# Kernel optimization log

Hardware: AMD Instinct MI355X
Metric: run time of the kernel (lower is better)

Reference implementation:

```python
import jax, jax.numpy as jnp
import numpy as np

N_NODES = 40000
N_EDGES = 640000
IN_CH = 11
HID = 128
OUT_CH = 1
NUM_LEVELS = 2


def _lin(x, w, b):
    # torch nn.Linear: w is [out, in]
    return x @ w.T + b


def _conv(x, src, dst, w1, b1, w2, b2, w3, b3):
    # Reconstructed MLMPNNConv forward: embed, then NUM_LEVELS rounds of
    # scatter-add message passing (message = x_j), concat levels, project.
    h = jax.nn.relu(_lin(x, w1, b1))  # [N, HID]
    outs = []
    for _ in range(NUM_LEVELS):
        agg = jax.ops.segment_sum(h[src], dst, num_segments=N_NODES)  # gather + scatter-add
        h = jax.nn.relu(_lin(agg, w2, b2))
        outs.append(h)
    return _lin(jnp.concatenate(outs, axis=-1), w3, b3)  # [N, out]


def setup_inputs() -> dict:
    key = jax.random.key(0)
    ks = jax.random.split(key, 16)
    d = {}
    d["x"] = jax.random.normal(ks[0], (N_NODES, IN_CH), dtype=jnp.float32)
    d["edge_index"] = jax.random.randint(ks[1], (2, N_EDGES), 0, N_NODES, dtype=jnp.int32)
    s = 0.05
    # conv 0: lin1 IN->HID, lin2 HID->HID, lin3 2*HID->HID
    d["c0_w1"] = jax.random.normal(ks[2], (HID, IN_CH)) * s
    d["c0_b1"] = jnp.zeros((HID,), jnp.float32)
    d["c0_w2"] = jax.random.normal(ks[3], (HID, HID)) * s
    d["c0_b2"] = jnp.zeros((HID,), jnp.float32)
    d["c0_w3"] = jax.random.normal(ks[4], (HID, HID * NUM_LEVELS)) * s
    d["c0_b3"] = jnp.zeros((HID,), jnp.float32)
    # conv 1: lin1 HID->HID
    d["c1_w1"] = jax.random.normal(ks[5], (HID, HID)) * s
    d["c1_b1"] = jnp.zeros((HID,), jnp.float32)
    d["c1_w2"] = jax.random.normal(ks[6], (HID, HID)) * s
    d["c1_b2"] = jnp.zeros((HID,), jnp.float32)
    d["c1_w3"] = jax.random.normal(ks[7], (HID, HID * NUM_LEVELS)) * s
    d["c1_b3"] = jnp.zeros((HID,), jnp.float32)
    # head
    d["f_w1"] = jax.random.normal(ks[8], (HID, HID)) * s
    d["f_b1"] = jnp.zeros((HID,), jnp.float32)
    d["f_w2"] = jax.random.normal(ks[9], (OUT_CH, HID)) * s
    d["f_b2"] = jnp.zeros((OUT_CH,), jnp.float32)
    return d


def reference(x, edge_index,
              c0_w1, c0_b1, c0_w2, c0_b2, c0_w3, c0_b3,
              c1_w1, c1_b1, c1_w2, c1_b2, c1_w3, c1_b3,
              f_w1, f_b1, f_w2, f_b2):
    src, dst = edge_index[0], edge_index[1]
    h = _conv(x, src, dst, c0_w1, c0_b1, c0_w2, c0_b2, c0_w3, c0_b3)
    h = _conv(h, src, dst, c1_w1, c1_b1, c1_w2, c1_b2, c1_w3, c1_b3)
    h = jax.nn.relu(_lin(h, f_w1, f_b1))
    return _lin(h, f_w2, f_b2)  # [N, 1]
```

## Files before the change

### kernel.cpp

```cpp
#include <hip/hip_runtime.h>
#include <hip/hip_fp16.h>

#define NN 40000
#define NE 640000
#define HID 128
#define SCAN_BLK ((NN + 255) / 256)
#define EB ((NE + 255) / 256)
#define ECAP 1536

typedef __attribute__((ext_vector_type(8)))  short short8;
typedef __attribute__((ext_vector_type(4)))  short short4v;
typedef __attribute__((ext_vector_type(16))) float floatx16;
typedef unsigned int uint;

__device__ __forceinline__ short f2bf(float f) {
    union { float f; unsigned u; } c; c.f = f;
    unsigned u = c.u;
    unsigned r = (u + 0x7FFF + ((u >> 16) & 1)) >> 16;
    return (short)r;
}
__device__ __forceinline__ float bf2f(short h) {
    union { unsigned u; float f; } c;
    c.u = ((unsigned)(unsigned short)h) << 16;
    return c.f;
}
__device__ __forceinline__ float2 h2f2(uint u) {
    union { uint u; __half2 h; } c; c.u = u;
    return __half22float2(c.h);
}
__device__ __forceinline__ void splits(float f, short* hi, short* lo) {
    short h = f2bf(f);
    *hi = h;
    *lo = f2bf(f - bf2f(h));
}
__device__ __forceinline__ void unpack8(uint4 a, uint4 b, short8* h, short8* l) {
    short8 H, L;
    H[0] = (short)(a.x >> 16); L[0] = (short)a.x;
    H[1] = (short)(a.y >> 16); L[1] = (short)a.y;
    H[2] = (short)(a.z >> 16); L[2] = (short)a.z;
    H[3] = (short)(a.w >> 16); L[3] = (short)a.w;
    H[4] = (short)(b.x >> 16); L[4] = (short)b.x;
    H[5] = (short)(b.y >> 16); L[5] = (short)b.y;
    H[6] = (short)(b.z >> 16); L[6] = (short)b.z;
    H[7] = (short)(b.w >> 16); L[7] = (short)b.w;
    *h = H; *l = L;
}

__device__ __forceinline__ int wswz(int o, int k) {
    int chunk = k >> 4, half = (k >> 3) & 1, j = k & 7;
    int ct = o >> 5, m31 = o & 31;
    int lane = half * 32 + m31;
    return (((chunk * 4 + ct) * 64 + lane) * 8 + j);
}

#define ACC4(u, A, B)                                                     \
    { float2 f0 = h2f2(u.x), f1 = h2f2(u.y);                              \
      float2 f2 = h2f2(u.z), f3 = h2f2(u.w);                              \
      A.x += f0.x; A.y += f0.y; A.z += f1.x; A.w += f1.y;                 \
      B.x += f2.x; B.y += f2.y; B.z += f3.x; B.w += f3.y; }

#define GBODY(IDX)                                                        \
        for (; e + 8 <= hi; e += 8) {                                     \
            int s0 = IDX(e + sub);     int s1 = IDX(e + 2 + sub);         \
            int s2 = IDX(e + 4 + sub); int s3 = IDX(e + 6 + sub);         \
            uint4 u0 = hp[(size_t)s0 * 16 + c16];                         \
            uint4 u1 = hp[(size_t)s1 * 16 + c16];                         \
            uint4 u2 = hp[(size_t)s2 * 16 + c16];                         \
            uint4 u3 = hp[(size_t)s3 * 16 + c16];                         \
            ACC4(u0, a0, a1); ACC4(u1, b0, b1);                           \
            ACC4(u2, c0, c1); ACC4(u3, d0, d1);                           \
        }                                                                 \
        for (; e + 2 <= hi; e += 2) {                                     \
            int s0 = IDX(e + sub);                                        \
            uint4 u0 = hp[(size_t)s0 * 16 + c16];                         \
            ACC4(u0, a0, a1);                                             \
        }                                                                 \
        if (sub == 0 && e < hi) {                                         \
            int s0 = IDX(e);                                              \
            uint4 u0 = hp[(size_t)s0 * 16 + c16];                         \
            ACC4(u0, b0, b1);                                             \
        }

#define IDXS(j) sE[(j)]
#define IDXG(j) esrc[lo0 + (j)]

__global__ __launch_bounds__(256, 4) void fused_gather_lin_kernel(
    const __half* __restrict__ h, const int* __restrict__ row_ptr,
    const int* __restrict__ esrc, const uint* __restrict__ Wq,
    const float* __restrict__ bias, __half* __restrict__ out)
{
    __shared__ short sAh[4096];
    __shared__ short sAl[4096];
    __shared__ int   sE[ECAP];
    __shared__ int   sRP[33];
    __shared__ int   sCtr;
    const int t   = threadIdx.x;
    const int r0  = blockIdx.x * 32;
    const int c16 = t & 15;
    const int sub = (t >> 4) & 1;
    const uint4* hp = (const uint4*)h;

    if (t == 0) sCtr = 0;
    if (t < 33) sRP[t] = row_ptr[r0 + t];
    __syncthreads();
    const int lo0 = sRP[0];
    const int nE  = sRP[32] - lo0;
    const int nStage = nE < ECAP ? nE : ECAP;
    for (int i = t; i < nStage; i += 256) sE[i] = esrc[lo0 + i];
    __syncthreads();
    const bool fast = (nE <= ECAP);

    for (;;) {
        int n = 0;
        if ((t & 31) == 0) n = atomicAdd(&sCtr, 1);
        n = __shfl(n, 0, 32);
        if (n >= 32) break;
        const int lo = sRP[n] - lo0, hi = sRP[n + 1] - lo0;
        float4 a0 = make_float4(0,0,0,0), a1 = make_float4(0,0,0,0);
        float4 b0 = make_float4(0,0,0,0), b1 = make_float4(0,0,0,0);
        float4 c0 = make_float4(0,0,0,0), c1 = make_float4(0,0,0,0);
        float4 d0 = make_float4(0,0,0,0), d1 = make_float4(0,0,0,0);
        int e = lo;
        if (fast) { GBODY(IDXS) } else { GBODY(IDXG) }
        float4 v0, v1;
        v0.x = (a0.x + b0.x) + (c0.x + d0.x);
        v0.y = (a0.y + b0.y) + (c0.y + d0.y);
        v0.z = (a0.z + b0.z) + (c0.z + d0.z);
        v0.w = (a0.w + b0.w) + (c0.w + d0.w);
        v1.x = (a1.x + b1.x) + (c1.x + d1.x);
        v1.y = (a1.y + b1.y) + (c1.y + d1.y);
        v1.z = (a1.z + b1.z) + (c1.z + d1.z);
        v1.w = (a1.w + b1.w) + (c1.w + d1.w);
        v0.x += __shfl_down(v0.x, 16, 32);
        v0.y += __shfl_down(v0.y, 16, 32);
        v0.z += __shfl_down(v0.z, 16, 32);
        v0.w += __shfl_down(v0.w, 16, 32);
        v1.x += __shfl_down(v1.x, 16, 32);
        v1.y += __shfl_down(v1.y, 16, 32);
        v1.z += __shfl_down(v1.z, 16, 32);
        v1.w += __shfl_down(v1.w, 16, 32);
        if (sub == 0) {
            short8 H, L;
            short hh, ll;
            splits(v0.x, &hh, &ll); H[0] = hh; L[0] = ll;
            splits(v0.y, &hh, &ll); H[1] = hh; L[1] = ll;
            splits(v0.z, &hh, &ll); H[2] = hh; L[2] = ll;
            splits(v0.w, &hh, &ll); H[3] = hh; L[3] = ll;
            splits(v1.x, &hh, &ll); H[4] = hh; L[4] = ll;
            splits(v1.y, &hh, &ll); H[5] = hh; L[5] = ll;
            splits(v1.z, &hh, &ll); H[6] = hh; L[6] = ll;
            splits(v1.w, &hh, &ll); H[7] = hh; L[7] = ll;
            const int off = c16 * 256 + n * 8;
            *(short8*)(sAh + off) = H;
            *(short8*)(sAl + off) = L;
        }
    }
    __syncthreads();

    const int wv   = t >> 6;
    const int lane = t & 63;
    const int m31  = lane & 31;
    const int half = lane >> 5;
    floatx16 acc;
    #pragma unroll
    for (int i = 0; i < 16; ++i) acc[i] = 0.f;
    #pragma unroll
    for (int c = 0; c < 8; ++c) {
        short8 ah = *(const short8*)(sAh + (c * 2 + half) * 256 + m31 * 8);
        short8 al = *(const short8*)(sAl + (c * 2 + half) * 256 + m31 * 8);
        const uint* wr = Wq + ((size_t)(c * 4 + wv) * 64 + lane) * 8;
        uint4 w0 = *(const uint4*)(wr);
        uint4 w1 = *(const uint4*)(wr + 4);
        short8 bh, bl;
        unpack8(w0, w1, &bh, &bl);
        acc = __builtin_amdgcn_mfma_f32_32x32x16_bf16(ah, bh, acc, 0, 0, 0);
        acc = __builtin_amdgcn_mfma_f32_32x32x16_bf16(al, bh, acc, 0, 0, 0);
        acc = __builtin_amdgcn_mfma_f32_32x32x16_bf16(ah, bl, acc, 0, 0, 0);
    }
    const int col = wv * 32 + m31;
    const float bb = bias[col];
    #pragma unroll
    for (int reg = 0; reg < 16; ++reg) {
        int row = (reg & 3) + 8 * (reg >> 2) + 4 * half;
        float v = fmaxf(acc[reg] + bb, 0.f);
        out[(size_t)(r0 + row) * HID + col] = __float2half(v);
    }
}

template<int PHASES, bool RELU>
__global__ __launch_bounds__(256, 4) void lin32_kernel(
    const __half* __restrict__ X0, const __half* __restrict__ X1,
    const uint* __restrict__ Wq, const float* __restrict__ bias,
    __half* __restrict__ out)
{
    __shared__ short sAh[PHASES * 4096];
    __shared__ short sAl[PHASES * 4096];
    const int t  = threadIdx.x;
    const int r0 = blockIdx.x * 32;

    #pragma unroll
    for (int i = 0; i < PHASES * 4; ++i) {
        int v = t + 256 * i;
        const __half* Xp = (PHASES == 2 && v >= 1024) ? X1 : X0;
        int vv  = v & 1023;
        int row = vv >> 5, q = vv & 31;
        uint2 u = *(const uint2*)(Xp + (size_t)(r0 + row) * 128 + q * 4);
        float2 f0 = h2f2(u.x), f1 = h2f2(u.y);
        int kk  = ((PHASES == 2) ? (v >> 10) * 128 : 0) + q * 4;
        int off = (kk >> 3) * 256 + row * 8 + (q & 1) * 4;
        short4v hi, lo;
        short hh, ll;
        splits(f0.x, &hh, &ll); hi.x = hh; lo.x = ll;
        splits(f0.y, &hh, &ll); hi.y = hh; lo.y = ll;
        splits(f1.x, &hh, &ll); hi.z = hh; lo.z = ll;
        splits(f1.y, &hh, &ll); hi.w = hh; lo.w = ll;
        *(short4v*)(sAh + off) = hi;
        *(short4v*)(sAl + off) = lo;
    }
    __syncthreads();

    const int wv   = t >> 6;
    const int lane = t & 63;
    const int m31  = lane & 31;
    const int half = lane >> 5;
    floatx16 acc;
    #pragma unroll
    for (int i = 0; i < 16; ++i) acc[i] = 0.f;
    #pragma unroll
    for (int c = 0; c < PHASES * 8; ++c) {
        short8 ah = *(const short8*)(sAh + (c * 2 + half) * 256 + m31 * 8);
        short8 al = *(const short8*)(sAl + (c * 2 + half) * 256 + m31 * 8);
        const uint* wr = Wq + ((size_t)(c * 4 + wv) * 64 + lane) * 8;
        uint4 w0 = *(const uint4*)(wr);
        uint4 w1 = *(const uint4*)(wr + 4);
        short8 bh, bl;
        unpack8(w0, w1, &bh, &bl);
        acc = __builtin_amdgcn_mfma_f32_32x32x16_bf16(ah, bh, acc, 0, 0, 0);
        acc = __builtin_amdgcn_mfma_f32_32x32x16_bf16(al, bh, acc, 0, 0, 0);
        acc = __builtin_amdgcn_mfma_f32_32x32x16_bf16(ah, bl, acc, 0, 0, 0);
    }
    const int col = wv * 32 + m31;
    const float bb = bias[col];
    #pragma unroll
    for (int reg = 0; reg < 16; ++reg) {
        int row = (reg & 3) + 8 * (reg >> 2) + 4 * half;
        float v = acc[reg] + bb;
        if (RELU) v = fmaxf(v, 0.f);
        out[(size_t)(r0 + row) * HID + col] = __float2half(v);
    }
}

__global__ __launch_bounds__(256, 3) void cat_head_kernel(
    const __half* __restrict__ X0, const __half* __restrict__ X1,
    const uint* __restrict__ Wq, const float* __restrict__ bias,
    const float* __restrict__ f2, const float* __restrict__ f2b,
    float* __restrict__ out)
{
    __shared__ short sAh[8192];
    __shared__ short sAl[8192];
    __shared__ float gbuf[32 * 129];
    const int t  = threadIdx.x;
    const int r0 = blockIdx.x * 32;

    #pragma unroll
    for (int i = 0; i < 8; ++i) {
        int v = t + 256 * i;
        const __half* Xp = (v >= 1024) ? X1 : X0;
        int vv  = v & 1023;
        int row = vv >> 5, q = vv & 31;
        uint2 u = *(const uint2*)(Xp + (size_t)(r0 + row) * 128 + q * 4);
        float2 f0 = h2f2(u.x), f1 = h2f2(u.y);
        int kk  = (v >> 10) * 128 + q * 4;
        int off = (kk >> 3) * 256 + row * 8 + (q & 1) * 4;
        short4v hi, lo;
        short hh, ll;
        splits(f0.x, &hh, &ll); hi.x = hh; lo.x = ll;
        splits(f0.y, &hh, &ll); hi.y = hh; lo.y = ll;
        splits(f1.x, &hh, &ll); hi.z = hh; lo.z = ll;
        splits(f1.y, &hh, &ll); hi.w = hh; lo.w = ll;
        *(short4v*)(sAh + off) = hi;
        *(short4v*)(sAl + off) = lo;
    }
    __syncthreads();

    const int wv   = t >> 6;
    const int lane = t & 63;
    const int m31  = lane & 31;
    const int half = lane >> 5;
    floatx16 acc;
    #pragma unroll
    for (int i = 0; i < 16; ++i) acc[i] = 0.f;
    #pragma unroll
    for (int c = 0; c < 16; ++c) {
        short8 ah = *(const short8*)(sAh + (c * 2 + half) * 256 + m31 * 8);
        short8 al = *(const short8*)(sAl + (c * 2 + half) * 256 + m31 * 8);
        const uint* wr = Wq + ((size_t)(c * 4 + wv) * 64 + lane) * 8;
        uint4 w0 = *(const uint4*)(wr);
        uint4 w1 = *(const uint4*)(wr + 4);
        short8 bh, bl;
        unpack8(w0, w1, &bh, &bl);
        acc = __builtin_amdgcn_mfma_f32_32x32x16_bf16(ah, bh, acc, 0, 0, 0);
        acc = __builtin_amdgcn_mfma_f32_32x32x16_bf16(al, bh, acc, 0, 0, 0);
        acc = __builtin_amdgcn_mfma_f32_32x32x16_bf16(ah, bl, acc, 0, 0, 0);
    }
    const int col = wv * 32 + m31;
    const float bb = bias[col];
    #pragma unroll
    for (int reg = 0; reg < 16; ++reg) {
        int row = (reg & 3) + 8 * (reg >> 2) + 4 * half;
        gbuf[row * 129 + col] = fmaxf(acc[reg] + bb, 0.f);
    }
    __syncthreads();

    const int node = t >> 3;
    const int seg  = t & 7;
    const float* gr = gbuf + node * 129 + seg * 16;
    float a = 0.f;
    #pragma unroll
    for (int i = 0; i < 16; ++i) a += gr[i] * f2[seg * 16 + i];
    a += __shfl_down(a, 4, 8);
    a += __shfl_down(a, 2, 8);
    a += __shfl_down(a, 1, 8);
    if (seg == 0) out[r0 + node] = a + f2b[0];
}

__global__ __launch_bounds__(256) void prep_kernel(
    const float* __restrict__ c0w2, const float* __restrict__ c1w2,
    const float* __restrict__ c1w1, const float* __restrict__ c0w3,
    const float* __restrict__ c0b3, const float* __restrict__ c1b1,
    const float* __restrict__ fw1,  const float* __restrict__ c1w3,
    const float* __restrict__ c1b3, const float* __restrict__ fb1,
    const int* __restrict__ dst, int* __restrict__ cnt,
    uint* __restrict__ wp, uint* __restrict__ p_Wa, uint* __restrict__ p_Wb,
    float* __restrict__ f_ba, float* __restrict__ f_bb)
{
    const int b = blockIdx.x;
    const int t = threadIdx.x;
    if (b < 128) {
        int i = b * 256 + t;
        const float* src = (i < 16384) ? c0w2 : c1w2;
        int off = (i < 16384) ? 0 : 16384;
        int L = i - off;
        int o = L >> 7, k = L & 127;
        short hh, ll;
        splits(src[L], &hh, &ll);
        wp[off + wswz(o, k)] = ((uint)(unsigned short)hh << 16) | (uint)(unsigned short)ll;
    } else if (b < 384) {
        const bool isA = (b < 256);
        const int o = b - (isA ? 128 : 256);
        const float* A   = isA ? c1w1 : fw1;
        const float* B   = isA ? c0w3 : c1w3;
        const float* bi  = isA ? c0b3 : c1b3;
        const float* bo  = isA ? c1b1 : fb1;
        uint*  W  = isA ? p_Wa : p_Wb;
        float* bb = isA ? f_ba : f_bb;
        const float* Ar = A + o * 128;
        float s = 0.f;
        for (int j = 0; j < 128; ++j) s += Ar[j] * B[j * 256 + t];
        short hh, ll;
        splits(s, &hh, &ll);
        W[wswz(o, t)] = ((uint)(unsigned short)hh << 16) | (uint)(unsigned short)ll;
        if (t == 0) {
            float sb = 0.f;
            for (int j = 0; j < 128; ++j) sb += Ar[j] * bi[j];
            bb[o] = sb + bo[o];
        }
    } else {
        int e = (b - 384) * 256 + t;
        if (e < NE) atomicAdd(&cnt[dst[e]], 1);
    }
}

__global__ __launch_bounds__(256) void scan1_kernel(
    const int* __restrict__ cnt, int* __restrict__ row_ptr,
    int* __restrict__ partials)
{
    __shared__ int s[256];
    const int t = threadIdx.x;
    const int i = blockIdx.x * 256 + t;
    int v = (i < NN) ? cnt[i] : 0;
    s[t] = v;
    __syncthreads();
    #pragma unroll
    for (int off = 1; off < 256; off <<= 1) {
        int x = (t >= off) ? s[t - off] : 0;
        __syncthreads();
        s[t] += x;
        __syncthreads();
    }
    if (i < NN) row_ptr[i] = s[t] - v;
    if (t == 255) partials[blockIdx.x] = s[255];
}

__global__ __launch_bounds__(256) void scan2_kernel(
    int* __restrict__ partials, int* __restrict__ row_ptr)
{
    __shared__ int s[256];
    const int t = threadIdx.x;
    int v = (t < SCAN_BLK) ? partials[t] : 0;
    s[t] = v;
    __syncthreads();
    #pragma unroll
    for (int off = 1; off < 256; off <<= 1) {
        int x = (t >= off) ? s[t - off] : 0;
        __syncthreads();
        s[t] += x;
        __syncthreads();
    }
    if (t < SCAN_BLK) partials[t] = s[t] - v;
    if (t == 255) row_ptr[NN] = s[255];
}

__global__ __launch_bounds__(256) void scan3_kernel(
    int* __restrict__ row_ptr, const int* __restrict__ partials)
{
    const int i = blockIdx.x * 256 + threadIdx.x;
    if (i < NN) row_ptr[i] += partials[blockIdx.x];
}

__global__ __launch_bounds__(256) void fill_embed_kernel(
    const int* __restrict__ src, const int* __restrict__ dst,
    const int* __restrict__ row_ptr, int* __restrict__ pos,
    int* __restrict__ esrc,
    const float* __restrict__ x, const float* __restrict__ w1,
    const float* __restrict__ b1, __half* __restrict__ h0)
{
    const int b = blockIdx.x;
    const int t = threadIdx.x;
    if (b < EB) {
        int e = b * 256 + t;
        if (e < NE) {
            int d = dst[e];
            int p = row_ptr[d] + atomicAdd(&pos[d], 1);
            esrc[p] = src[e];
        }
    } else {
        __shared__ float xs[2][88];
        const int hf = t >> 7;
        const int m  = t & 127;
        const int r0 = (b - EB) * 16 + hf * 8;
        for (int i = m; i < 88; i += 128) {
            int r = i / 11, k = i - r * 11;
            xs[hf][i] = x[(size_t)(r0 + r) * 11 + k];
        }
        __syncthreads();
        float acc[8] = {};
        const float* Wm = w1 + m * 11;
        #pragma unroll
        for (int k = 0; k < 11; ++k) {
            float w = Wm[k];
            #pragma unroll
            for (int r = 0; r < 8; ++r) acc[r] += xs[hf][r * 11 + k] * w;
        }
        const float bias = b1[m];
        #pragma unroll
        for (int r = 0; r < 8; ++r) {
            float v = fmaxf(acc[r] + bias, 0.f);
            h0[(size_t)(r0 + r) * HID + m] = __float2half(v);
        }
    }
}

extern "C" void kernel_launch(void* const* d_in, const int* in_sizes, int n_in,
                              void* d_out, int out_size, void* d_ws, size_t ws_size,
                              hipStream_t stream)
{
    const float* x     = (const float*)d_in[0];
    const int*   eidx  = (const int*)d_in[1];
    const float* c0_w1 = (const float*)d_in[2],  *c0_b1 = (const float*)d_in[3];
    const float* c0_w2 = (const float*)d_in[4],  *c0_b2 = (const float*)d_in[5];
    const float* c0_w3 = (const float*)d_in[6],  *c0_b3 = (const float*)d_in[7];
    const float* c1_w1 = (const float*)d_in[8],  *c1_b1 = (const float*)d_in[9];
    const float* c1_w2 = (const float*)d_in[10], *c1_b2 = (const float*)d_in[11];
    const float* c1_w3 = (const float*)d_in[12], *c1_b3 = (const float*)d_in[13];
    const float* f_w1  = (const float*)d_in[14], *f_b1  = (const float*)d_in[15];
    const float* f_w2  = (const float*)d_in[16], *f_b2  = (const float*)d_in[17];
    const int* src = eidx;
    const int* dst = eidx + NE;
    float* out = (float*)d_out;

    const size_t BUF = (size_t)NN * HID;
    __half* bA = (__half*)d_ws;
    __half* bB = bA + BUF;
    __half* bC = bB + BUF;
    int* row_ptr  = (int*)(bC + BUF);
    int* cnt      = row_ptr + (NN + 1);
    int* pos      = cnt + NN;
    int* esrc     = pos + NN;
    int* partials = esrc + NE;
    uint* wp      = (uint*)(partials + SCAN_BLK);

    uint* p_c0w2 = wp + 0;
    uint* p_c1w2 = wp + 16384;
    uint* p_Wa   = wp + 32768;
    uint* p_Wb   = wp + 65536;
    float* f_ba  = (float*)(wp + 98304);
    float* f_bb  = f_ba + 128;

    const int nbl = (NN + 31) / 32;

    (void)hipMemsetAsync(cnt, 0, 2 * NN * sizeof(int), stream);
    prep_kernel<<<384 + EB, 256, 0, stream>>>(
        c0_w2, c1_w2, c1_w1, c0_w3, c0_b3, c1_b1,
        f_w1, c1_w3, c1_b3, f_b1, dst, cnt, wp, p_Wa, p_Wb, f_ba, f_bb);
    scan1_kernel<<<SCAN_BLK, 256, 0, stream>>>(cnt, row_ptr, partials);
    scan2_kernel<<<1, 256, 0, stream>>>(partials, row_ptr);
    scan3_kernel<<<SCAN_BLK, 256, 0, stream>>>(row_ptr, partials);
    fill_embed_kernel<<<EB + 2500, 256, 0, stream>>>(
        src, dst, row_ptr, pos, esrc, x, c0_w1, c0_b1, bA);

    fused_gather_lin_kernel<<<nbl, 256, 0, stream>>>(bA, row_ptr, esrc, p_c0w2, c0_b2, bB);
    fused_gather_lin_kernel<<<nbl, 256, 0, stream>>>(bB, row_ptr, esrc, p_c0w2, c0_b2, bC);
    lin32_kernel<2, true><<<nbl, 256, 0, stream>>>(bB, bC, p_Wa, f_ba, bA);

    fused_gather_lin_kernel<<<nbl, 256, 0, stream>>>(bA, row_ptr, esrc, p_c1w2, c1_b2, bB);
    fused_gather_lin_kernel<<<nbl, 256, 0, stream>>>(bB, row_ptr, esrc, p_c1w2, c1_b2, bC);
    cat_head_kernel<<<nbl, 256, 0, stream>>>(bB, bC, p_Wb, f_bb, f_w2, f_b2, out);
}
```

Baseline: 306.5 us.

## Merge three-pass scan into one block and record edge rank during counting

The three-kernel scan over node degrees becomes a single 1024-thread block scan, where each thread serially sums a chunk of 40 counts. The counting pass also stores the atomicAdd return value as a per-edge rank, so the CSR fill no longer needs a second atomic per edge or the pos array. This removes two kernel launches, one memset region and 640K contended atomics. In exchange it adds a 640K-int rank write and read, aliased into the bC buffer, and a serial single-block scan with strided, uncoalesced per-thread reads.

```diff
diff --git a/kernel.cpp b/kernel.cpp
--- a/kernel.cpp
+++ b/kernel.cpp
@@ -4,7 +4,6 @@
 #define NN 40000
 #define NE 640000
 #define HID 128
-#define SCAN_BLK ((NN + 255) / 256)
 #define EB ((NE + 255) / 256)
 #define ECAP 1536
 
@@ -330,7 +329,7 @@
     const float* __restrict__ c0b3, const float* __restrict__ c1b1,
     const float* __restrict__ fw1,  const float* __restrict__ c1w3,
     const float* __restrict__ c1b3, const float* __restrict__ fb1,
-    const int* __restrict__ dst, int* __restrict__ cnt,
+    const int* __restrict__ dst, int* __restrict__ cnt, int* __restrict__ rank,
     uint* __restrict__ wp, uint* __restrict__ p_Wa, uint* __restrict__ p_Wb,
     float* __restrict__ f_ba, float* __restrict__ f_bb)
 {
@@ -367,60 +366,47 @@
         }
     } else {
         int e = (b - 384) * 256 + t;
-        if (e < NE) atomicAdd(&cnt[dst[e]], 1);
-    }
-}
-
-__global__ __launch_bounds__(256) void scan1_kernel(
-    const int* __restrict__ cnt, int* __restrict__ row_ptr,
-    int* __restrict__ partials)
-{
-    __shared__ int s[256];
+        if (e < NE) rank[e] = atomicAdd(&cnt[dst[e]], 1);
+    }
+}
+
+#define SCHUNK 40
+__global__ __launch_bounds__(1024) void scan_kernel(
+    const int* __restrict__ cnt, int* __restrict__ row_ptr)
+{
+    __shared__ int s[1024];
     const int t = threadIdx.x;
-    const int i = blockIdx.x * 256 + t;
-    int v = (i < NN) ? cnt[i] : 0;
-    s[t] = v;
-    __syncthreads();
-    #pragma unroll
-    for (int off = 1; off < 256; off <<= 1) {
+    const int base = t * SCHUNK;
+    int sum = 0;
+    if (base < NN) {
+        int n = min(SCHUNK, NN - base);
+        #pragma unroll 8
+        for (int j = 0; j < n; ++j) sum += cnt[base + j];
+    }
+    s[t] = sum;
+    __syncthreads();
+    #pragma unroll
+    for (int off = 1; off < 1024; off <<= 1) {
         int x = (t >= off) ? s[t - off] : 0;
         __syncthreads();
         s[t] += x;
         __syncthreads();
     }
-    if (i < NN) row_ptr[i] = s[t] - v;
-    if (t == 255) partials[blockIdx.x] = s[255];
-}
-
-__global__ __launch_bounds__(256) void scan2_kernel(
-    int* __restrict__ partials, int* __restrict__ row_ptr)
-{
-    __shared__ int s[256];
-    const int t = threadIdx.x;
-    int v = (t < SCAN_BLK) ? partials[t] : 0;
-    s[t] = v;
-    __syncthreads();
-    #pragma unroll
-    for (int off = 1; off < 256; off <<= 1) {
-        int x = (t >= off) ? s[t - off] : 0;
-        __syncthreads();
-        s[t] += x;
-        __syncthreads();
-    }
-    if (t < SCAN_BLK) partials[t] = s[t] - v;
-    if (t == 255) row_ptr[NN] = s[255];
-}
-
-__global__ __launch_bounds__(256) void scan3_kernel(
-    int* __restrict__ row_ptr, const int* __restrict__ partials)
-{
-    const int i = blockIdx.x * 256 + threadIdx.x;
-    if (i < NN) row_ptr[i] += partials[blockIdx.x];
+    int run = (t == 0) ? 0 : s[t - 1];
+    if (base < NN) {
+        int n = min(SCHUNK, NN - base);
+        for (int j = 0; j < n; ++j) {
+            int v = cnt[base + j];
+            row_ptr[base + j] = run;
+            run += v;
+        }
+    }
+    if (t == 1023) row_ptr[NN] = s[1023];
 }
 
 __global__ __launch_bounds__(256) void fill_embed_kernel(
     const int* __restrict__ src, const int* __restrict__ dst,
-    const int* __restrict__ row_ptr, int* __restrict__ pos,
+    const int* __restrict__ row_ptr, const int* __restrict__ rank,
     int* __restrict__ esrc,
     const float* __restrict__ x, const float* __restrict__ w1,
     const float* __restrict__ b1, __half* __restrict__ h0)
@@ -431,8 +417,7 @@
         int e = b * 256 + t;
         if (e < NE) {
             int d = dst[e];
-            int p = row_ptr[d] + atomicAdd(&pos[d], 1);
-            esrc[p] = src[e];
+            esrc[row_ptr[d] + rank[e]] = src[e];
         }
     } else {
         __shared__ float xs[2][88];
@@ -485,10 +470,8 @@
     __half* bC = bB + BUF;
     int* row_ptr  = (int*)(bC + BUF);
     int* cnt      = row_ptr + (NN + 1);
-    int* pos      = cnt + NN;
-    int* esrc     = pos + NN;
-    int* partials = esrc + NE;
-    uint* wp      = (uint*)(partials + SCAN_BLK);
+    int* esrc     = cnt + NN;
+    uint* wp      = (uint*)(esrc + NE);
 
     uint* p_c0w2 = wp + 0;
     uint* p_c1w2 = wp + 16384;
@@ -497,17 +480,17 @@
     float* f_ba  = (float*)(wp + 98304);
     float* f_bb  = f_ba + 128;
 
+    int* rank = (int*)bC;
+
     const int nbl = (NN + 31) / 32;
 
-    (void)hipMemsetAsync(cnt, 0, 2 * NN * sizeof(int), stream);
+    (void)hipMemsetAsync(cnt, 0, NN * sizeof(int), stream);
     prep_kernel<<<384 + EB, 256, 0, stream>>>(
         c0_w2, c1_w2, c1_w1, c0_w3, c0_b3, c1_b1,
-        f_w1, c1_w3, c1_b3, f_b1, dst, cnt, wp, p_Wa, p_Wb, f_ba, f_bb);
-    scan1_kernel<<<SCAN_BLK, 256, 0, stream>>>(cnt, row_ptr, partials);
-    scan2_kernel<<<1, 256, 0, stream>>>(partials, row_ptr);
-    scan3_kernel<<<SCAN_BLK, 256, 0, stream>>>(row_ptr, partials);
+        f_w1, c1_w3, c1_b3, f_b1, dst, cnt, rank, wp, p_Wa, p_Wb, f_ba, f_bb);
+    scan_kernel<<<1, 1024, 0, stream>>>(cnt, row_ptr);
     fill_embed_kernel<<<EB + 2500, 256, 0, stream>>>(
-        src, dst, row_ptr, pos, esrc, x, c0_w1, c0_b1, bA);
+        src, dst, row_ptr, rank, esrc, x, c0_w1, c0_b1, bA);
 
     fused_gather_lin_kernel<<<nbl, 256, 0, stream>>>(bA, row_ptr, esrc, p_c0w2, c0_b2, bB);
     fused_gather_lin_kernel<<<nbl, 256, 0, stream>>>(bB, row_ptr, esrc, p_c0w2, c0_b2, bC);
```

Result: faster. 298.7 us (-2.6%).
